# Performance work log

Measured on AMD Instinct MI355X. Metric: run time of the kernel, lower is better.

Reference implementation:

```python
import jax, jax.numpy as jnp
import numpy as np

B, L, H, VOC, OUT = 64, 512, 64, 32000, 5


def setup_inputs() -> dict:
    key = jax.random.key(0)
    ks = jax.random.split(key, 7)
    tokens = jax.random.randint(ks[0], (B, L), 0, VOC, dtype=jnp.int32)
    embed = jax.random.normal(ks[1], (VOC, H), dtype=jnp.float32) * 0.1
    V = jax.random.normal(ks[2], (H, 2 * H, 2 * H), dtype=jnp.float32) * 0.05
    W = jax.random.normal(ks[3], (2 * H, H), dtype=jnp.float32) * 0.05
    b = jax.random.normal(ks[4], (1, H), dtype=jnp.float32) * 0.05
    Wout = jax.random.normal(ks[5], (H, OUT), dtype=jnp.float32) * 0.05
    bout = jax.random.normal(ks[6], (OUT,), dtype=jnp.float32) * 0.05
    return {"tokens": tokens, "embed": embed, "V": V, "W": W, "b": b,
            "Wout": Wout, "bout": bout}


def _combine(c, V, W, b):
    # c: [B, N, 2H] concatenated (left, right) children.
    # xVx[b,n,i] = c[b,n] @ V[i] @ c[b,n]^T  (RNTN bilinear term)
    xVx = jnp.einsum('bnp,ipq,bnq->bni', c, V, c)
    Wx = jnp.einsum('bnp,ph->bnh', c, W)
    return jnp.tanh(xVx + Wx + b)  # b broadcasts [1,H] -> [B,N,H]


def reference(tokens, embed, V, W, b, Wout, bout):
    # Leaves: embedding lookup, [B, L, H]
    nodes = embed[tokens]
    # Complete binary tree: combine adjacent pairs level by level
    # (fixed log2(L)=9 levels -> static shapes, jit friendly)
    while nodes.shape[1] > 1:
        left = nodes[:, 0::2]   # [B, N/2, H]
        right = nodes[:, 1::2]  # [B, N/2, H]
        c = jnp.concatenate([left, right], axis=-1)  # [B, N/2, 2H]
        nodes = _combine(c, V, W, b)
    root = nodes[:, 0]  # [B, H]
    logits = root @ Wout + bout
    return jax.nn.log_softmax(logits, axis=-1)
```

## Files before the change

### kernel.cpp

```cpp
#include <hip/hip_runtime.h>
#include <cmath>

static constexpr int kB = 64, kL = 512, kH = 64, kH2 = 128, kOut = 5;

typedef short bf16x8 __attribute__((ext_vector_type(8)));
typedef float f32x4  __attribute__((ext_vector_type(4)));

__device__ __forceinline__ unsigned short f2bf(float f) {
  unsigned u = __float_as_uint(f);
  unsigned r = (u + 0x7FFFu + ((u >> 16) & 1u)) >> 16;
  return (unsigned short)r;
}

__device__ __forceinline__ void cvt8(const f32x4& v0, const f32x4& v1,
                                     bf16x8& hi, bf16x8& lo) {
  #pragma unroll
  for (int j = 0; j < 4; ++j) {
    unsigned short h0 = f2bf(v0[j]);
    unsigned short h1 = f2bf(v1[j]);
    hi[j]     = (short)h0;
    hi[j + 4] = (short)h1;
    lo[j]     = (short)f2bf(v0[j] - __uint_as_float(((unsigned)h0) << 16));
    lo[j + 4] = (short)f2bf(v1[j] - __uint_as_float(((unsigned)h1) << 16));
  }
}

__global__ void prep_k(const float* __restrict__ V, const float* __restrict__ W,
                       unsigned short* __restrict__ vhi, unsigned short* __restrict__ wt) {
  int idx = blockIdx.x * 256 + threadIdx.x;
  if (idx < kH * kH2 * kH2) {
    vhi[idx] = f2bf(V[idx]);
  } else {
    int widx = idx - kH * kH2 * kH2;
    if (widx < kH * kH2) {
      int i = widx >> 7, p = widx & 127;
      wt[widx] = f2bf(W[p * kH + i]);
    }
  }
}

template<bool FIRST>
__global__ __launch_bounds__(256) void combine2_k(
    const float* __restrict__ in, const int* __restrict__ tokens,
    const float* __restrict__ embed, const unsigned short* __restrict__ vhi,
    const unsigned short* __restrict__ wt, const float* __restrict__ bias,
    float* __restrict__ out, int M, int IS)
{
  __shared__ unsigned short Vs[2][kH2 * kH2];
  __shared__ float res[128 * 17];

  const int t = threadIdx.x;
  const int lane = t & 63, w = t >> 6;
  const int c = lane & 15, q = lane >> 4;
  const int m0 = (int)blockIdx.x * 128;
  const int i0 = (int)blockIdx.y * IS;
  const int Mrows = (M < 128) ? M : 128;
  const bool has_rows = (w * 32) < Mrows;

  bf16x8 bh[2][4], bl[2][4];
  f32x4  Cred[2][8];

  if (has_rows) {
    #pragma unroll
    for (int mt = 0; mt < 2; ++mt) {
      int m = m0 + w * 32 + mt * 16 + c;
      const float* crow = nullptr;
      int tokA = 0, tokB = 0;
      if (FIRST) {
        int b = m >> 8, j = m & 255;
        tokA = tokens[b * kL + 2 * j];
        tokB = tokens[b * kL + 2 * j + 1];
      } else {
        crow = in + (size_t)m * kH2;
      }
      #pragma unroll
      for (int ks = 0; ks < 4; ++ks) {
        int q0 = ks * 32 + q * 8;
        const float* src = FIRST
            ? (embed + (size_t)(q0 < 64 ? tokA : tokB) * kH + (q0 & 63))
            : (crow + q0);
        f32x4 v0 = *(const f32x4*)src;
        f32x4 v1 = *(const f32x4*)(src + 4);
        cvt8(v0, v1, bh[mt][ks], bl[mt][ks]);
      }
      #pragma unroll
      for (int pt = 0; pt < 8; ++pt) {
        int p0 = pt * 16 + q * 4;
        const float* src = FIRST
            ? (embed + (size_t)(p0 < 64 ? tokA : tokB) * kH + (p0 & 63))
            : (crow + p0);
        Cred[mt][pt] = *(const f32x4*)src;
      }
    }
    {
      int irow = i0 + c; if (irow > 63) irow = 63;
      f32x4 ah0 = {0.f,0.f,0.f,0.f}, al0 = ah0, ah1 = ah0, al1 = ah0;
      #pragma unroll
      for (int ks = 0; ks < 4; ++ks) {
        bf16x8 a = *(const bf16x8*)(wt + (size_t)irow * kH2 + ks * 32 + q * 8);
        ah0 = __builtin_amdgcn_mfma_f32_16x16x32_bf16(a, bh[0][ks], ah0, 0, 0, 0);
        al0 = __builtin_amdgcn_mfma_f32_16x16x32_bf16(a, bl[0][ks], al0, 0, 0, 0);
        ah1 = __builtin_amdgcn_mfma_f32_16x16x32_bf16(a, bh[1][ks], ah1, 0, 0, 0);
        al1 = __builtin_amdgcn_mfma_f32_16x16x32_bf16(a, bl[1][ks], al1, 0, 0, 0);
      }
      #pragma unroll
      for (int reg = 0; reg < 4; ++reg) {
        int ii = q * 4 + reg;
        if (ii < IS) {
          float bv = bias[i0 + ii];
          res[(w * 32 + c) * 17 + ii]      = ah0[reg] + al0[reg] + bv;
          res[(w * 32 + 16 + c) * 17 + ii] = ah1[reg] + al1[reg] + bv;
        }
      }
    }
  }

  auto stageV = [&](int i, int buf) {
    const unsigned short* vsrc = vhi + (size_t)i * (kH2 * kH2);
    #pragma unroll
    for (int r = 0; r < 8; ++r) {
      int chunk = w * 512 + r * 64 + lane;
      int p  = chunk >> 4;
      int pc = chunk & 15;
      int cc = pc ^ (p & 7);
      const unsigned short* g = vsrc + p * kH2 + cc * 8;
      __builtin_amdgcn_global_load_lds(
          (const __attribute__((address_space(1))) unsigned int*)g,
          (__attribute__((address_space(3))) unsigned int*)
              ((char*)&Vs[buf][0] + (size_t)(w * 512 + r * 64) * 16),
          16, 0, 0);
    }
  };

  auto computeIC = [&](int ic, int buf) {
    const char* vbase = (const char*)&Vs[buf][0];
    float g0 = 0.f, g1 = 0.f;
    for (int pt = 0; pt < 8; ++pt) {
      f32x4 a0 = {0.f,0.f,0.f,0.f}, a2 = a0;
      #pragma unroll
      for (int ks = 0; ks < 4; ++ks) {
        int p  = pt * 16 + c;
        int cc = (ks * 4 + q) ^ (p & 7);
        bf16x8 vf = *(const bf16x8*)(vbase + (size_t)p * 256 + cc * 16);
        a0 = __builtin_amdgcn_mfma_f32_16x16x32_bf16(vf, bh[0][ks], a0, 0, 0, 0);
        a2 = __builtin_amdgcn_mfma_f32_16x16x32_bf16(vf, bh[1][ks], a2, 0, 0, 0);
      }
      f32x4 cr0 = Cred[0][pt], cr1 = Cred[1][pt];
      g0 = fmaf(cr0[0], a0[0], g0); g0 = fmaf(cr0[1], a0[1], g0);
      g0 = fmaf(cr0[2], a0[2], g0); g0 = fmaf(cr0[3], a0[3], g0);
      g1 = fmaf(cr1[0], a2[0], g1); g1 = fmaf(cr1[1], a2[1], g1);
      g1 = fmaf(cr1[2], a2[2], g1); g1 = fmaf(cr1[3], a2[3], g1);
    }
    g0 += __shfl_xor(g0, 16); g0 += __shfl_xor(g0, 32);
    g1 += __shfl_xor(g1, 16); g1 += __shfl_xor(g1, 32);
    if (q == 0)      res[(w * 32 + c) * 17 + ic]      += g0;
    else if (q == 1) res[(w * 32 + 16 + c) * 17 + ic] += g1;
  };

  if (IS >= 2) {
    stageV(i0, 0); stageV(i0 + 1, 1);
    __syncthreads();
    for (int icp = 0; icp < IS; icp += 2) {
      if (has_rows) {
        computeIC(icp, 0);
        computeIC(icp + 1, 1);
      }
      __syncthreads();
      if (icp + 2 < IS) {
        stageV(i0 + icp + 2, 0); stageV(i0 + icp + 3, 1);
        __syncthreads();
      }
    }
  } else {
    stageV(i0, 0);
    __syncthreads();
    if (has_rows) computeIC(0, 0);
    __syncthreads();
  }

  const int sh = __builtin_ctz(IS);
  for (int idx = t; idx < Mrows * IS; idx += 256) {
    int m = idx >> sh, ii = idx & (IS - 1);
    out[(size_t)(m0 + m) * kH + i0 + ii] = tanhf(res[m * 17 + ii]);
  }
}

__global__ void head_k(const float* __restrict__ root,
                       const float* __restrict__ Wout,
                       const float* __restrict__ bout,
                       float* __restrict__ out) {
  int b = threadIdx.x;
  float l[kOut];
  #pragma unroll
  for (int o = 0; o < kOut; ++o) l[o] = bout[o];
  for (int h = 0; h < kH; ++h) {
    float r = root[b * kH + h];
    #pragma unroll
    for (int o = 0; o < kOut; ++o) l[o] = fmaf(r, Wout[h * kOut + o], l[o]);
  }
  float mx = l[0];
  #pragma unroll
  for (int o = 1; o < kOut; ++o) mx = fmaxf(mx, l[o]);
  float s = 0.f;
  #pragma unroll
  for (int o = 0; o < kOut; ++o) s += expf(l[o] - mx);
  float lse = logf(s);
  #pragma unroll
  for (int o = 0; o < kOut; ++o) out[b * kOut + o] = l[o] - mx - lse;
}

extern "C" void kernel_launch(void* const* d_in, const int* in_sizes, int n_in,
                              void* d_out, int out_size, void* d_ws, size_t ws_size,
                              hipStream_t stream) {
  const int*   tokens = (const int*)  d_in[0];
  const float* embed  = (const float*)d_in[1];
  const float* V      = (const float*)d_in[2];
  const float* W      = (const float*)d_in[3];
  const float* bias   = (const float*)d_in[4];
  const float* Wout   = (const float*)d_in[5];
  const float* bout   = (const float*)d_in[6];
  float* out = (float*)d_out;

  char* ws = (char*)d_ws;
  unsigned short* vhi = (unsigned short*)ws;
  unsigned short* wt  = (unsigned short*)(ws + 2097152);
  float* bufA = (float*)(ws + 2097152 + 16384);
  float* bufB = (float*)(ws + 2097152 + 16384 + 4194304);

  int nprep = kH * kH2 * kH2 + kH * kH2;
  prep_k<<<dim3((nprep + 255) / 256), 256, 0, stream>>>(V, W, vhi, wt);

  const float* cur = nullptr;
  float* nxt = bufA;
  bool first = true;
  for (int Nout = 256; Nout >= 1; Nout >>= 1) {
    int M = kB * Nout;
    int gx = (M + 127) / 128;
    int IS = gx / 8; if (IS < 1) IS = 1; if (IS > 16) IS = 16;
    dim3 grid(gx, 64 / IS);
    if (first)
      combine2_k<true ><<<grid, 256, 0, stream>>>(nullptr, tokens, embed, vhi, wt, bias, nxt, M, IS);
    else
      combine2_k<false><<<grid, 256, 0, stream>>>(cur, nullptr, nullptr, vhi, wt, bias, nxt, M, IS);
    first = false;
    cur = nxt;
    nxt = (nxt == bufA) ? bufB : bufA;
  }
  head_k<<<1, 64, 0, stream>>>(cur, Wout, bout, out);
}
```

Measured before the change: 216.5 us.

## Split bilinear reduction across 8 waves by K-half and P-half with LDS atomics

Doubles the block to 512 threads and regroups waves into 2 row groups of 64 rows, with each wave owning half of the K dimension and half of the P dimension of the V contraction. Partial quadratic-form sums are combined in shared memory with atomicAdd. Only one wave per row group computes the W·x linear term, which drops the per-wave bl registers. The aim is lower register pressure per wave and more waves in flight for the MFMA work, at the cost of LDS atomic contention and an imbalance where one wave does extra linear-term work.

New measurement: 444.2 us. 105% more time.

```diff
diff --git a/kernel.cpp b/kernel.cpp
--- a/kernel.cpp
+++ b/kernel.cpp
@@ -40,7 +40,7 @@
 }
 
 template<bool FIRST>
-__global__ __launch_bounds__(256) void combine2_k(
+__global__ __launch_bounds__(512, 4) void combine2_k(
     const float* __restrict__ in, const int* __restrict__ tokens,
     const float* __restrict__ embed, const unsigned short* __restrict__ vhi,
     const unsigned short* __restrict__ wt, const float* __restrict__ bias,
@@ -52,18 +52,22 @@
   const int t = threadIdx.x;
   const int lane = t & 63, w = t >> 6;
   const int c = lane & 15, q = lane >> 4;
+  const int kh = w & 1;
+  const int ph = (w >> 1) & 1;
+  const int mg = w >> 2;
   const int m0 = (int)blockIdx.x * 128;
   const int i0 = (int)blockIdx.y * IS;
   const int Mrows = (M < 128) ? M : 128;
-  const bool has_rows = (w * 32) < Mrows;
-
-  bf16x8 bh[2][4], bl[2][4];
-  f32x4  Cred[2][8];
+  const bool has_rows = (mg * 64) < Mrows;
+  const bool dw = (kh == 0) && (ph == 0);
+
+  bf16x8 bh[4][2];
+  f32x4  Cred[4][4];
 
   if (has_rows) {
     #pragma unroll
-    for (int mt = 0; mt < 2; ++mt) {
-      int m = m0 + w * 32 + mt * 16 + c;
+    for (int mt = 0; mt < 4; ++mt) {
+      int m = m0 + mg * 64 + mt * 16 + c;
       const float* crow = nullptr;
       int tokA = 0, tokB = 0;
       if (FIRST) {
@@ -73,44 +77,54 @@
       } else {
         crow = in + (size_t)m * kH2;
       }
+      if (dw) {
+        bf16x8 h4[4], l4[4];
+        #pragma unroll
+        for (int ks = 0; ks < 4; ++ks) {
+          int q0 = ks * 32 + q * 8;
+          const float* src = FIRST
+              ? (embed + (size_t)(q0 < 64 ? tokA : tokB) * kH + (q0 & 63))
+              : (crow + q0);
+          f32x4 v0 = *(const f32x4*)src;
+          f32x4 v1 = *(const f32x4*)(src + 4);
+          cvt8(v0, v1, h4[ks], l4[ks]);
+        }
+        int irow = i0 + c; if (irow > 63) irow = 63;
+        f32x4 ah = {0.f,0.f,0.f,0.f}, al = ah;
+        #pragma unroll
+        for (int ks = 0; ks < 4; ++ks) {
+          bf16x8 a = *(const bf16x8*)(wt + (size_t)irow * kH2 + ks * 32 + q * 8);
+          ah = __builtin_amdgcn_mfma_f32_16x16x32_bf16(a, h4[ks], ah, 0, 0, 0);
+          al = __builtin_amdgcn_mfma_f32_16x16x32_bf16(a, l4[ks], al, 0, 0, 0);
+        }
+        #pragma unroll
+        for (int reg = 0; reg < 4; ++reg) {
+          int ii = q * 4 + reg;
+          if (ii < IS)
+            res[(mg * 64 + mt * 16 + c) * 17 + ii] = ah[reg] + al[reg] + bias[i0 + ii];
+        }
+        bh[mt][0] = h4[0]; bh[mt][1] = h4[1];
+      } else {
+        #pragma unroll
+        for (int ksl = 0; ksl < 2; ++ksl) {
+          int ks = kh * 2 + ksl;
+          int q0 = ks * 32 + q * 8;
+          const float* src = FIRST
+              ? (embed + (size_t)(q0 < 64 ? tokA : tokB) * kH + (q0 & 63))
+              : (crow + q0);
+          f32x4 v0 = *(const f32x4*)src;
+          f32x4 v1 = *(const f32x4*)(src + 4);
+          bf16x8 lo_dummy;
+          cvt8(v0, v1, bh[mt][ksl], lo_dummy);
+        }
+      }
       #pragma unroll
-      for (int ks = 0; ks < 4; ++ks) {
-        int q0 = ks * 32 + q * 8;
-        const float* src = FIRST
-            ? (embed + (size_t)(q0 < 64 ? tokA : tokB) * kH + (q0 & 63))
-            : (crow + q0);
-        f32x4 v0 = *(const f32x4*)src;
-        f32x4 v1 = *(const f32x4*)(src + 4);
-        cvt8(v0, v1, bh[mt][ks], bl[mt][ks]);
-      }
-      #pragma unroll
-      for (int pt = 0; pt < 8; ++pt) {
-        int p0 = pt * 16 + q * 4;
+      for (int ptl = 0; ptl < 4; ++ptl) {
+        int p0 = (ph * 4 + ptl) * 16 + q * 4;
         const float* src = FIRST
             ? (embed + (size_t)(p0 < 64 ? tokA : tokB) * kH + (p0 & 63))
             : (crow + p0);
-        Cred[mt][pt] = *(const f32x4*)src;
-      }
-    }
-    {
-      int irow = i0 + c; if (irow > 63) irow = 63;
-      f32x4 ah0 = {0.f,0.f,0.f,0.f}, al0 = ah0, ah1 = ah0, al1 = ah0;
-      #pragma unroll
-      for (int ks = 0; ks < 4; ++ks) {
-        bf16x8 a = *(const bf16x8*)(wt + (size_t)irow * kH2 + ks * 32 + q * 8);
-        ah0 = __builtin_amdgcn_mfma_f32_16x16x32_bf16(a, bh[0][ks], ah0, 0, 0, 0);
-        al0 = __builtin_amdgcn_mfma_f32_16x16x32_bf16(a, bl[0][ks], al0, 0, 0, 0);
-        ah1 = __builtin_amdgcn_mfma_f32_16x16x32_bf16(a, bh[1][ks], ah1, 0, 0, 0);
-        al1 = __builtin_amdgcn_mfma_f32_16x16x32_bf16(a, bl[1][ks], al1, 0, 0, 0);
-      }
-      #pragma unroll
-      for (int reg = 0; reg < 4; ++reg) {
-        int ii = q * 4 + reg;
-        if (ii < IS) {
-          float bv = bias[i0 + ii];
-          res[(w * 32 + c) * 17 + ii]      = ah0[reg] + al0[reg] + bv;
-          res[(w * 32 + 16 + c) * 17 + ii] = ah1[reg] + al1[reg] + bv;
-        }
+        Cred[mt][ptl] = *(const f32x4*)src;
       }
     }
   }
@@ -118,8 +132,8 @@
   auto stageV = [&](int i, int buf) {
     const unsigned short* vsrc = vhi + (size_t)i * (kH2 * kH2);
     #pragma unroll
-    for (int r = 0; r < 8; ++r) {
-      int chunk = w * 512 + r * 64 + lane;
+    for (int r = 0; r < 4; ++r) {
+      int chunk = w * 256 + r * 64 + lane;
       int p  = chunk >> 4;
       int pc = chunk & 15;
       int cc = pc ^ (p & 7);
@@ -127,34 +141,44 @@
       __builtin_amdgcn_global_load_lds(
           (const __attribute__((address_space(1))) unsigned int*)g,
           (__attribute__((address_space(3))) unsigned int*)
-              ((char*)&Vs[buf][0] + (size_t)(w * 512 + r * 64) * 16),
+              ((char*)&Vs[buf][0] + (size_t)chunk * 16),
           16, 0, 0);
     }
   };
 
   auto computeIC = [&](int ic, int buf) {
     const char* vbase = (const char*)&Vs[buf][0];
-    float g0 = 0.f, g1 = 0.f;
-    for (int pt = 0; pt < 8; ++pt) {
-      f32x4 a0 = {0.f,0.f,0.f,0.f}, a2 = a0;
+    float g0 = 0.f, g1 = 0.f, g2 = 0.f, g3 = 0.f;
+    #pragma unroll
+    for (int ptl = 0; ptl < 4; ++ptl) {
+      int p = (ph * 4 + ptl) * 16 + c;
+      f32x4 a0 = {0.f,0.f,0.f,0.f}, a1 = a0, a2 = a0, a3 = a0;
       #pragma unroll
-      for (int ks = 0; ks < 4; ++ks) {
-        int p  = pt * 16 + c;
+      for (int ksl = 0; ksl < 2; ++ksl) {
+        int ks = kh * 2 + ksl;
         int cc = (ks * 4 + q) ^ (p & 7);
         bf16x8 vf = *(const bf16x8*)(vbase + (size_t)p * 256 + cc * 16);
-        a0 = __builtin_amdgcn_mfma_f32_16x16x32_bf16(vf, bh[0][ks], a0, 0, 0, 0);
-        a2 = __builtin_amdgcn_mfma_f32_16x16x32_bf16(vf, bh[1][ks], a2, 0, 0, 0);
-      }
-      f32x4 cr0 = Cred[0][pt], cr1 = Cred[1][pt];
-      g0 = fmaf(cr0[0], a0[0], g0); g0 = fmaf(cr0[1], a0[1], g0);
-      g0 = fmaf(cr0[2], a0[2], g0); g0 = fmaf(cr0[3], a0[3], g0);
-      g1 = fmaf(cr1[0], a2[0], g1); g1 = fmaf(cr1[1], a2[1], g1);
-      g1 = fmaf(cr1[2], a2[2], g1); g1 = fmaf(cr1[3], a2[3], g1);
+        a0 = __builtin_amdgcn_mfma_f32_16x16x32_bf16(vf, bh[0][ksl], a0, 0, 0, 0);
+        a1 = __builtin_amdgcn_mfma_f32_16x16x32_bf16(vf, bh[1][ksl], a1, 0, 0, 0);
+        a2 = __builtin_amdgcn_mfma_f32_16x16x32_bf16(vf, bh[2][ksl], a2, 0, 0, 0);
+        a3 = __builtin_amdgcn_mfma_f32_16x16x32_bf16(vf, bh[3][ksl], a3, 0, 0, 0);
+      }
+      f32x4 c0 = Cred[0][ptl], c1 = Cred[1][ptl], c2 = Cred[2][ptl], c3 = Cred[3][ptl];
+      g0 = fmaf(c0[0], a0[0], g0); g0 = fmaf(c0[1], a0[1], g0);
+      g0 = fmaf(c0[2], a0[2], g0); g0 = fmaf(c0[3], a0[3], g0);
+      g1 = fmaf(c1[0], a1[0], g1); g1 = fmaf(c1[1], a1[1], g1);
+      g1 = fmaf(c1[2], a1[2], g1); g1 = fmaf(c1[3], a1[3], g1);
+      g2 = fmaf(c2[0], a2[0], g2); g2 = fmaf(c2[1], a2[1], g2);
+      g2 = fmaf(c2[2], a2[2], g2); g2 = fmaf(c2[3], a2[3], g2);
+      g3 = fmaf(c3[0], a3[0], g3); g3 = fmaf(c3[1], a3[1], g3);
+      g3 = fmaf(c3[2], a3[2], g3); g3 = fmaf(c3[3], a3[3], g3);
     }
     g0 += __shfl_xor(g0, 16); g0 += __shfl_xor(g0, 32);
     g1 += __shfl_xor(g1, 16); g1 += __shfl_xor(g1, 32);
-    if (q == 0)      res[(w * 32 + c) * 17 + ic]      += g0;
-    else if (q == 1) res[(w * 32 + 16 + c) * 17 + ic] += g1;
+    g2 += __shfl_xor(g2, 16); g2 += __shfl_xor(g2, 32);
+    g3 += __shfl_xor(g3, 16); g3 += __shfl_xor(g3, 32);
+    float gq = (q == 0) ? g0 : (q == 1) ? g1 : (q == 2) ? g2 : g3;
+    atomicAdd(&res[(mg * 64 + q * 16 + c) * 17 + ic], gq);
   };
 
   if (IS >= 2) {
@@ -179,7 +203,7 @@
   }
 
   const int sh = __builtin_ctz(IS);
-  for (int idx = t; idx < Mrows * IS; idx += 256) {
+  for (int idx = t; idx < Mrows * IS; idx += 512) {
     int m = idx >> sh, ii = idx & (IS - 1);
     out[(size_t)(m0 + m) * kH + i0 + ii] = tanhf(res[m * 17 + ii]);
   }
@@ -239,9 +263,9 @@
     int IS = gx / 8; if (IS < 1) IS = 1; if (IS > 16) IS = 16;
     dim3 grid(gx, 64 / IS);
     if (first)
-      combine2_k<true ><<<grid, 256, 0, stream>>>(nullptr, tokens, embed, vhi, wt, bias, nxt, M, IS);
+      combine2_k<true ><<<grid, 512, 0, stream>>>(nullptr, tokens, embed, vhi, wt, bias, nxt, M, IS);
     else
-      combine2_k<false><<<grid, 256, 0, stream>>>(cur, nullptr, nullptr, vhi, wt, bias, nxt, M, IS);
+      combine2_k<false><<<grid, 512, 0, stream>>>(cur, nullptr, nullptr, vhi, wt, bias, nxt, M, IS);
     first = false;
     cur = nxt;
     nxt = (nxt == bufA) ? bufB : bufA;
```

## Drop bf16 lo-split for Wx term and store bf16 activation copies

Applied to the files above, without the earlier changes.

Removes the hi/lo bf16 split of the child vectors: the W projection now uses only the bf16-rounded inputs, which halves its MFMAs and removes the in-kernel conversion. The prep kernel now also converts the whole embedding table to bf16. Each level writes a bf16 copy of its output alongside the fp32 one, so the next level can load bf16 fragments directly. In exchange, the extra embedding conversion (32000x64) adds prep work and memory traffic, the extra bf16 stores add write bandwidth, and the Wx term loses precision.

After: 205.7 us. -5.0%, faster.

```diff
diff --git a/kernel.cpp b/kernel.cpp
--- a/kernel.cpp
+++ b/kernel.cpp
@@ -1,7 +1,7 @@
 #include <hip/hip_runtime.h>
 #include <cmath>
 
-static constexpr int kB = 64, kL = 512, kH = 64, kH2 = 128, kOut = 5;
+static constexpr int kB = 64, kL = 512, kH = 64, kH2 = 128, kOut = 5, kVoc = 32000;
 
 typedef short bf16x8 __attribute__((ext_vector_type(8)));
 typedef float f32x4  __attribute__((ext_vector_type(4)));
@@ -12,39 +12,29 @@
   return (unsigned short)r;
 }
 
-__device__ __forceinline__ void cvt8(const f32x4& v0, const f32x4& v1,
-                                     bf16x8& hi, bf16x8& lo) {
-  #pragma unroll
-  for (int j = 0; j < 4; ++j) {
-    unsigned short h0 = f2bf(v0[j]);
-    unsigned short h1 = f2bf(v1[j]);
-    hi[j]     = (short)h0;
-    hi[j + 4] = (short)h1;
-    lo[j]     = (short)f2bf(v0[j] - __uint_as_float(((unsigned)h0) << 16));
-    lo[j + 4] = (short)f2bf(v1[j] - __uint_as_float(((unsigned)h1) << 16));
-  }
-}
-
 __global__ void prep_k(const float* __restrict__ V, const float* __restrict__ W,
-                       unsigned short* __restrict__ vhi, unsigned short* __restrict__ wt) {
+                       const float* __restrict__ embed,
+                       unsigned short* __restrict__ vhi, unsigned short* __restrict__ wt,
+                       unsigned short* __restrict__ ebf) {
   int idx = blockIdx.x * 256 + threadIdx.x;
-  if (idx < kH * kH2 * kH2) {
-    vhi[idx] = f2bf(V[idx]);
-  } else {
-    int widx = idx - kH * kH2 * kH2;
-    if (widx < kH * kH2) {
-      int i = widx >> 7, p = widx & 127;
-      wt[widx] = f2bf(W[p * kH + i]);
-    }
-  }
+  if (idx < kH * kH2 * kH2) { vhi[idx] = f2bf(V[idx]); return; }
+  idx -= kH * kH2 * kH2;
+  if (idx < kH * kH2) {
+    int i = idx >> 7, p = idx & 127;
+    wt[idx] = f2bf(W[p * kH + i]);
+    return;
+  }
+  idx -= kH * kH2;
+  if (idx < kVoc * kH) ebf[idx] = f2bf(embed[idx]);
 }
 
 template<bool FIRST>
 __global__ __launch_bounds__(256) void combine2_k(
-    const float* __restrict__ in, const int* __restrict__ tokens,
-    const float* __restrict__ embed, const unsigned short* __restrict__ vhi,
-    const unsigned short* __restrict__ wt, const float* __restrict__ bias,
-    float* __restrict__ out, int M, int IS)
+    const float* __restrict__ in, const unsigned short* __restrict__ inbf,
+    const int* __restrict__ tokens, const float* __restrict__ embed,
+    const unsigned short* __restrict__ vhi, const unsigned short* __restrict__ wt,
+    const float* __restrict__ bias, float* __restrict__ out,
+    unsigned short* __restrict__ outbf, int M, int IS)
 {
   __shared__ unsigned short Vs[2][kH2 * kH2];
   __shared__ float res[128 * 17];
@@ -57,7 +47,7 @@
   const int Mrows = (M < 128) ? M : 128;
   const bool has_rows = (w * 32) < Mrows;
 
-  bf16x8 bh[2][4], bl[2][4];
+  bf16x8 bh[2][4];
   f32x4  Cred[2][8];
 
   if (has_rows) {
@@ -65,6 +55,7 @@
     for (int mt = 0; mt < 2; ++mt) {
       int m = m0 + w * 32 + mt * 16 + c;
       const float* crow = nullptr;
+      const unsigned short* brow = nullptr;
       int tokA = 0, tokB = 0;
       if (FIRST) {
         int b = m >> 8, j = m & 255;
@@ -72,16 +63,15 @@
         tokB = tokens[b * kL + 2 * j + 1];
       } else {
         crow = in + (size_t)m * kH2;
+        brow = inbf + (size_t)m * kH2;
       }
       #pragma unroll
       for (int ks = 0; ks < 4; ++ks) {
         int q0 = ks * 32 + q * 8;
-        const float* src = FIRST
-            ? (embed + (size_t)(q0 < 64 ? tokA : tokB) * kH + (q0 & 63))
-            : (crow + q0);
-        f32x4 v0 = *(const f32x4*)src;
-        f32x4 v1 = *(const f32x4*)(src + 4);
-        cvt8(v0, v1, bh[mt][ks], bl[mt][ks]);
+        const unsigned short* bsrc = FIRST
+            ? (inbf + (size_t)(q0 < 64 ? tokA : tokB) * kH + (q0 & 63))
+            : (brow + q0);
+        bh[mt][ks] = *(const bf16x8*)bsrc;
       }
       #pragma unroll
       for (int pt = 0; pt < 8; ++pt) {
@@ -94,22 +84,20 @@
     }
     {
       int irow = i0 + c; if (irow > 63) irow = 63;
-      f32x4 ah0 = {0.f,0.f,0.f,0.f}, al0 = ah0, ah1 = ah0, al1 = ah0;
+      f32x4 ah0 = {0.f,0.f,0.f,0.f}, ah1 = ah0;
       #pragma unroll
       for (int ks = 0; ks < 4; ++ks) {
         bf16x8 a = *(const bf16x8*)(wt + (size_t)irow * kH2 + ks * 32 + q * 8);
         ah0 = __builtin_amdgcn_mfma_f32_16x16x32_bf16(a, bh[0][ks], ah0, 0, 0, 0);
-        al0 = __builtin_amdgcn_mfma_f32_16x16x32_bf16(a, bl[0][ks], al0, 0, 0, 0);
         ah1 = __builtin_amdgcn_mfma_f32_16x16x32_bf16(a, bh[1][ks], ah1, 0, 0, 0);
-        al1 = __builtin_amdgcn_mfma_f32_16x16x32_bf16(a, bl[1][ks], al1, 0, 0, 0);
       }
       #pragma unroll
       for (int reg = 0; reg < 4; ++reg) {
         int ii = q * 4 + reg;
         if (ii < IS) {
           float bv = bias[i0 + ii];
-          res[(w * 32 + c) * 17 + ii]      = ah0[reg] + al0[reg] + bv;
-          res[(w * 32 + 16 + c) * 17 + ii] = ah1[reg] + al1[reg] + bv;
+          res[(w * 32 + c) * 17 + ii]      = ah0[reg] + bv;
+          res[(w * 32 + 16 + c) * 17 + ii] = ah1[reg] + bv;
         }
       }
     }
@@ -181,7 +169,10 @@
   const int sh = __builtin_ctz(IS);
   for (int idx = t; idx < Mrows * IS; idx += 256) {
     int m = idx >> sh, ii = idx & (IS - 1);
-    out[(size_t)(m0 + m) * kH + i0 + ii] = tanhf(res[m * 17 + ii]);
+    float v = tanhf(res[m * 17 + ii]);
+    size_t o = (size_t)(m0 + m) * kH + i0 + ii;
+    out[o] = v;
+    outbf[o] = f2bf(v);
   }
 }
 
@@ -224,14 +215,19 @@
   char* ws = (char*)d_ws;
   unsigned short* vhi = (unsigned short*)ws;
   unsigned short* wt  = (unsigned short*)(ws + 2097152);
-  float* bufA = (float*)(ws + 2097152 + 16384);
-  float* bufB = (float*)(ws + 2097152 + 16384 + 4194304);
-
-  int nprep = kH * kH2 * kH2 + kH * kH2;
-  prep_k<<<dim3((nprep + 255) / 256), 256, 0, stream>>>(V, W, vhi, wt);
+  unsigned short* ebf = (unsigned short*)(ws + 2097152 + 16384);
+  float* bufA = (float*)(ws + 2097152 + 16384 + 4194304);
+  float* bufB = (float*)(ws + 2097152 + 16384 + 4194304 + 4194304);
+  unsigned short* bfA = (unsigned short*)(ws + 2097152 + 16384 + 4194304 + 4194304 + 2097152);
+  unsigned short* bfB = (unsigned short*)(ws + 2097152 + 16384 + 4194304 + 4194304 + 2097152 + 2097152);
+
+  int nprep = kH * kH2 * kH2 + kH * kH2 + kVoc * kH;
+  prep_k<<<dim3((nprep + 255) / 256), 256, 0, stream>>>(V, W, embed, vhi, wt, ebf);
 
   const float* cur = nullptr;
+  const unsigned short* curbf = nullptr;
   float* nxt = bufA;
+  unsigned short* nxtbf = bfA;
   bool first = true;
   for (int Nout = 256; Nout >= 1; Nout >>= 1) {
     int M = kB * Nout;
@@ -239,12 +235,15 @@
     int IS = gx / 8; if (IS < 1) IS = 1; if (IS > 16) IS = 16;
     dim3 grid(gx, 64 / IS);
     if (first)
-      combine2_k<true ><<<grid, 256, 0, stream>>>(nullptr, tokens, embed, vhi, wt, bias, nxt, M, IS);
+      combine2_k<true ><<<grid, 256, 0, stream>>>(nullptr, ebf, tokens, embed,
+                                                  vhi, wt, bias, nxt, nxtbf, M, IS);
     else
-      combine2_k<false><<<grid, 256, 0, stream>>>(cur, nullptr, nullptr, vhi, wt, bias, nxt, M, IS);
+      combine2_k<false><<<grid, 256, 0, stream>>>(cur, curbf, nullptr, nullptr,
+                                                  vhi, wt, bias, nxt, nxtbf, M, IS);
     first = false;
-    cur = nxt;
-    nxt = (nxt == bufA) ? bufB : bufA;
+    cur = nxt; curbf = nxtbf;
+    nxt   = (nxt == bufA) ? bufB : bufA;
+    nxtbf = (nxtbf == bfA) ? bfB : bfA;
   }
   head_k<<<1, 64, 0, stream>>>(cur, Wout, bout, out);
 }
```
